# Kernel tuning notes

Hardware: AMD Instinct MI355X
Metric: run time of the kernel (lower is better)

The kernel has to match this reference:

```python
import jax, jax.numpy as jnp
import numpy as np

V, D, H, S = 100000, 300, 300, 4096   # vocab, embed dim, biLSTM hidden (2x150), seq len
HU = H // 2                            # per-direction LSTM units
NSYN = 4


def _lstm(x, W, U, b):
    """Keras-style LSTM scan. x: [S, D] -> hidden states [S, HU]. Gate order i,f,g,o."""
    def step(carry, xt):
        h, c = carry
        z = xt @ W + h @ U + b              # [4*HU]
        i, f, g, o = jnp.split(z, 4)
        i = jax.nn.sigmoid(i)
        f = jax.nn.sigmoid(f)
        g = jnp.tanh(g)
        o = jax.nn.sigmoid(o)
        c = f * c + i * g
        h = o * jnp.tanh(c)
        return (h, c), h
    init = (jnp.zeros((HU,), x.dtype), jnp.zeros((HU,), x.dtype))
    _, hs = jax.lax.scan(step, init, x)
    return hs


def setup_inputs() -> dict:
    key = jax.random.key(0)
    ks = jax.random.split(key, 20)
    s = 0.05  # small init scale keeps exp() attention scores well-conditioned
    return {
        "sentence": jax.random.randint(ks[0], (S,), 0, V),
        "synonym_indices": jax.random.randint(ks[1], (S, NSYN), 0, V),
        "embedding_matrix": jax.random.normal(ks[2], (V, D), jnp.float32) * s,
        # forward-direction LSTM
        "W_f": jax.random.normal(ks[3], (D, 4 * HU), jnp.float32) * s,
        "U_f": jax.random.normal(ks[4], (HU, 4 * HU), jnp.float32) * s,
        "b_f": jnp.zeros((4 * HU,), jnp.float32),
        # backward-direction LSTM
        "W_b": jax.random.normal(ks[5], (D, 4 * HU), jnp.float32) * s,
        "U_b": jax.random.normal(ks[6], (HU, 4 * HU), jnp.float32) * s,
        "b_b": jnp.zeros((4 * HU,), jnp.float32),
        # primary attention dense (h1 -> h1)
        "W_p": jax.random.normal(ks[7], (H, H), jnp.float32) * s,
        "b_p": jnp.zeros((H,), jnp.float32),
        # secondary attention dense (2*h1 -> 1, tanh)
        "W_s": jax.random.normal(ks[8], (2 * H, 1), jnp.float32) * s,
        "b_s": jnp.zeros((1,), jnp.float32),
        # output heads
        "W_emo": jax.random.normal(ks[9], (2 * H, 8), jnp.float32) * s,
        "b_emo": jnp.zeros((8,), jnp.float32),
        "W_sent": jax.random.normal(ks[10], (2 * H, 1), jnp.float32) * s,
        "b_sent": jnp.zeros((1,), jnp.float32),
    }


def reference(sentence, synonym_indices, embedding_matrix,
              W_f, U_f, b_f, W_b, U_b, b_b,
              W_p, b_p, W_s, b_s, W_emo, b_emo, W_sent, b_sent):
    emb = embedding_matrix[sentence]                       # [S, D] gather
    # bidirectional LSTM (concat fwd and reversed-bwd hidden states)
    h_fwd = _lstm(emb, W_f, U_f, b_f)                      # [S, HU]
    h_bwd = _lstm(emb[::-1], W_b, U_b, b_b)[::-1]          # [S, HU]
    hidden_states = jnp.concatenate([h_fwd, h_bwd], -1)    # [S, H]
    # primary attention: per-word synonym gather + exp-scored weighted sum (vectorized)
    out = hidden_states @ W_p + b_p                        # [S, H]
    syn = embedding_matrix[synonym_indices]                # [S, NSYN, D] irregular gather
    scores = jnp.exp(jnp.einsum('sd,skd->sk', out, syn))   # [S, NSYN]
    m = jnp.einsum('sk,skd->sd', scores, syn)              # [S, D]
    h_hats = jnp.concatenate([hidden_states, m], -1)       # [S, 2H]
    # secondary attention
    coeff = jnp.exp(jnp.tanh(h_hats @ W_s + b_s))          # [S, 1]
    H_HAT = jnp.sum(coeff * h_hats, axis=0)[None, :]       # [1, 2H]
    emotion_logits = H_HAT @ W_emo + b_emo                 # [1, 8]
    sentiment_logits = H_HAT @ W_sent + b_sent             # [1, 1]
    return (emotion_logits, sentiment_logits)
```

## Files before the change

### kernel.cpp

```cpp
#include <hip/hip_runtime.h>
#include <hip/hip_bf16.h>
#include <math.h>

#define S_LEN 4096
#define D_EMB 300
#define NG    600
#define HDIM  300
#define H2    600
#define VOCAB 100000

typedef float v4f __attribute__((ext_vector_type(4)));
typedef _Float16 f16x2 __attribute__((ext_vector_type(2)));
typedef _Float16 f16x8 __attribute__((ext_vector_type(8)));

__device__ __forceinline__ float bf2f(unsigned short u) {
  union { unsigned int i; float f; } v; v.i = ((unsigned int)u) << 16; return v.f;
}
__device__ __forceinline__ unsigned short f2bf(float f) {
  union { float f; unsigned int i; } v; v.f = f;
  return (unsigned short)((v.i + 0x7FFFu + ((v.i >> 16) & 1u)) >> 16);
}

__device__ __forceinline__ void bar_lds() {
  asm volatile("s_waitcnt lgkmcnt(0)\n\ts_barrier" ::: "memory");
}

__global__ void zero_hh(float* __restrict__ HH) {
  if (threadIdx.x < 640) HH[threadIdx.x] = 0.f;
}
__global__ void zero_out_f(float* __restrict__ o, int n) {
  if ((int)threadIdx.x < n) o[threadIdx.x] = 0.f;
}

#define BM 64
#define BN 64
#define BK 16
template<bool A_BF16>
__global__ __launch_bounds__(256) void gemm_bias(
    const void* __restrict__ Av,
    const int* __restrict__ idx, int lda, int nrowsA,
    const float* __restrict__ B,
    const float* __restrict__ bias,
    unsigned short* __restrict__ C,
    int N, int K)
{
  __shared__ __align__(16) float As[BK][BM + 4];
  __shared__ __align__(16) float Bs[BK][BN + 4];
  __shared__ int rowidx[BM];

  int tid = threadIdx.x;
  int bm0 = blockIdx.y * BM, bn0 = blockIdx.x * BN;
  if (tid < BM) {
    int r = idx ? idx[bm0 + tid] : (bm0 + tid);
    r = (r < 0) ? 0 : ((r >= nrowsA) ? (nrowsA - 1) : r);
    rowidx[tid] = r;
  }
  __syncthreads();

  int tx  = tid & 15, ty = tid >> 4;
  int ar  = tid >> 2, akv = (tid & 3) << 2;
  int bkr = tid >> 4, bnv = (tid & 15) << 2;

  float acc[4][4] = {};
  for (int kk = 0; kk < K; kk += BK) {
    float a0=0.f, a1=0.f, a2=0.f, a3=0.f;
    int ka = kk + akv;
    if (ka < K) {
      if (A_BF16) {
        const unsigned short* A = (const unsigned short*)Av;
        ushort4 qa = *(const ushort4*)(A + (size_t)rowidx[ar]*lda + ka);
        a0 = bf2f(qa.x); a1 = bf2f(qa.y); a2 = bf2f(qa.z); a3 = bf2f(qa.w);
      } else {
        const float* A = (const float*)Av;
        float4 qa = *(const float4*)(A + (size_t)rowidx[ar]*lda + ka);
        a0 = qa.x; a1 = qa.y; a2 = qa.z; a3 = qa.w;
      }
    }
    float b0=0.f, b1=0.f, b2=0.f, b3=0.f;
    int kb = kk + bkr, nb = bn0 + bnv;
    if (kb < K && nb < N) {
      float4 qb = *(const float4*)(B + (size_t)kb*N + nb);
      b0 = qb.x; b1 = qb.y; b2 = qb.z; b3 = qb.w;
    }
    As[akv+0][ar] = a0; As[akv+1][ar] = a1; As[akv+2][ar] = a2; As[akv+3][ar] = a3;
    Bs[bkr][bnv+0] = b0; Bs[bkr][bnv+1] = b1; Bs[bkr][bnv+2] = b2; Bs[bkr][bnv+3] = b3;
    __syncthreads();
    #pragma unroll
    for (int k = 0; k < BK; ++k) {
      v4f av = *(const v4f*)&As[k][ty << 2];
      v4f bv = *(const v4f*)&Bs[k][tx << 2];
      #pragma unroll
      for (int i = 0; i < 4; ++i)
        #pragma unroll
        for (int j = 0; j < 4; ++j)
          acc[i][j] += av[i] * bv[j];
    }
    __syncthreads();
  }
  #pragma unroll
  for (int i = 0; i < 4; ++i) {
    int m = bm0 + (ty << 2) + i;
    #pragma unroll
    for (int j = 0; j < 4; ++j) {
      int n = bn0 + (tx << 2) + j;
      if (n < N) C[(size_t)m*N + n] = f2bf(acc[i][j] + bias[n]);
    }
  }
}

__global__ __launch_bounds__(768) void lstm_kernel(
    const unsigned short* __restrict__ pre_f, const unsigned short* __restrict__ pre_b,
    const float* __restrict__ Uf, const float* __restrict__ Ub,
    unsigned short* __restrict__ hidden )
{
  const int dir = blockIdx.x;
  const unsigned short* pre = dir ? pre_b : pre_f;
  const float* U            = dir ? Ub : Uf;
  const int tid = threadIdx.x;

  __shared__ __align__(16) unsigned short h_u16[160];
  __shared__ __align__(16) float z2[3000];
  __shared__ __align__(16) float act[600];
  __shared__ __align__(16) float ring[3][600];
  __shared__ __align__(16) unsigned short h_hist[8][160];

  const bool faP = tid < 750;
  const int c4 = tid % 150, q = tid / 150;
  const int j0 = c4 << 2;
  const int k0 = q << 5;

  f16x2 u[4][16];
  if (faP) {
    #pragma unroll
    for (int cc = 0; cc < 4; ++cc)
      #pragma unroll
      for (int p = 0; p < 16; ++p) {
        int k = k0 + (p << 1);
        float a = (k     < 150) ? U[(size_t)k    *600 + j0 + cc] : 0.f;
        float b = (k + 1 < 150) ? U[(size_t)(k+1)*600 + j0 + cc] : 0.f;
        f16x2 v; v[0] = (_Float16)a; v[1] = (_Float16)b;
        u[cc][p] = v;
      }
  }

  int t  = dir ? (S_LEN - 1) : 0;
  const int dt = dir ? -1 : 1;

  if (tid < 160) h_u16[tid] = 0;
  unsigned short nxt1 = 0;
  if (tid < 600) {
    ring[0][tid] = bf2f(pre[(size_t)t*600 + tid]);
    nxt1 = pre[(size_t)(t + dt)*600 + tid];
  }
  float c = 0.f;
  __syncthreads();

  const _Float16* hf = (const _Float16*)h_u16;

  for (int s = 0; s < S_LEN; ++s) {
    if ((s & 7) == 0 && s) {
      if (tid < 600) {
        int sub = tid / 75, w = (tid % 75) << 1;
        int sp  = s - 8 + sub;
        int tp  = dir ? (S_LEN - 1 - sp) : sp;
        unsigned int v = *(const unsigned int*)&h_hist[sub][w];
        *(unsigned int*)(hidden + (size_t)tp*300 + dir*150 + w) = v;
      }
    }
    unsigned short nxt2 = 0;
    if (tid < 600 && s + 2 < S_LEN) nxt2 = pre[(size_t)(t + 2*dt)*600 + tid];

    if (faP) {
      f16x2 hp[16];
      *(f16x8*)&hp[0]  = *(const f16x8*)&hf[k0];
      *(f16x8*)&hp[4]  = *(const f16x8*)&hf[k0 + 8];
      *(f16x8*)&hp[8]  = *(const f16x8*)&hf[k0 + 16];
      *(f16x8*)&hp[12] = *(const f16x8*)&hf[k0 + 24];
      float a0 = 0.f, a1 = 0.f, a2 = 0.f, a3 = 0.f;
      #pragma unroll
      for (int p = 0; p < 16; ++p) {
        a0 = __builtin_amdgcn_fdot2(hp[p], u[0][p], a0, false);
        a1 = __builtin_amdgcn_fdot2(hp[p], u[1][p], a1, false);
        a2 = __builtin_amdgcn_fdot2(hp[p], u[2][p], a2, false);
        a3 = __builtin_amdgcn_fdot2(hp[p], u[3][p], a3, false);
      }
      v4f zp; zp[0] = a0; zp[1] = a1; zp[2] = a2; zp[3] = a3;
      *(v4f*)&z2[q*600 + j0] = zp;
    }
    if (tid < 600) ring[(s + 1) % 3][tid] = bf2f(nxt1);
    nxt1 = nxt2;
    bar_lds();

    if (tid < 600) {
      int j = tid;
      float z = ring[s % 3][j]
              + ((z2[j] + z2[600 + j]) + (z2[1200 + j] + z2[1800 + j]))
              + z2[2400 + j];
      bool is_g = (j >= 300) & (j < 450);
      float e = __expf(is_g ? (2.f * z) : (-z));
      float r = __builtin_amdgcn_rcpf(1.f + e);
      act[j] = is_g ? (1.f - 2.f * r) : r;
    }
    bar_lds();

    if (tid < 150) {
      float gi = act[tid], gf = act[150 + tid], gg = act[300 + tid], go = act[450 + tid];
      c = gf * c + gi * gg;
      float e = __expf(2.f * c);
      float th = 1.f - 2.f * __builtin_amdgcn_rcpf(e + 1.f);
      float hv = go * th;
      ((_Float16*)h_u16)[tid] = (_Float16)hv;
      h_hist[s & 7][tid] = f2bf(hv);
    }
    bar_lds();
    t += dt;
  }

  if (tid < 600) {
    int sub = tid / 75, w = (tid % 75) << 1;
    int sp  = S_LEN - 8 + sub;
    int tp  = dir ? (S_LEN - 1 - sp) : sp;
    unsigned int v = *(const unsigned int*)&h_hist[sub][w];
    *(unsigned int*)(hidden + (size_t)tp*300 + dir*150 + w) = v;
  }
}

__global__ __launch_bounds__(128) void attn_word(
    const unsigned short* __restrict__ outp,
    const unsigned short* __restrict__ hid,
    const float* __restrict__ E,
    const int* __restrict__ syn,
    const float* __restrict__ W_s,
    const float* __restrict__ b_s,
    float* __restrict__ HH)
{
  int t = blockIdx.x, tid = threadIdx.x;
  __shared__ float s_out[300], s_hid[300], s_syn[4][300], s_m[300];
  __shared__ float s_red[8], s_sc[4], s_cf;

  int r0 = syn[t*4+0], r1 = syn[t*4+1], r2 = syn[t*4+2], r3 = syn[t*4+3];
  r0 = (r0 < 0) ? 0 : ((r0 >= VOCAB) ? VOCAB-1 : r0);
  r1 = (r1 < 0) ? 0 : ((r1 >= VOCAB) ? VOCAB-1 : r1);
  r2 = (r2 < 0) ? 0 : ((r2 >= VOCAB) ? VOCAB-1 : r2);
  r3 = (r3 < 0) ? 0 : ((r3 >= VOCAB) ? VOCAB-1 : r3);
  for (int d = tid; d < 300; d += 128) {
    s_out[d] = bf2f(outp[(size_t)t*300 + d]);
    s_hid[d] = bf2f(hid[(size_t)t*300 + d]);
    s_syn[0][d] = E[(size_t)r0*300 + d];
    s_syn[1][d] = E[(size_t)r1*300 + d];
    s_syn[2][d] = E[(size_t)r2*300 + d];
    s_syn[3][d] = E[(size_t)r3*300 + d];
  }
  __syncthreads();

  float p0=0.f, p1=0.f, p2=0.f, p3=0.f;
  for (int d = tid; d < 300; d += 128) {
    float o = s_out[d];
    p0 += o*s_syn[0][d]; p1 += o*s_syn[1][d];
    p2 += o*s_syn[2][d]; p3 += o*s_syn[3][d];
  }
  #pragma unroll
  for (int off = 32; off; off >>= 1) {
    p0 += __shfl_down(p0, off); p1 += __shfl_down(p1, off);
    p2 += __shfl_down(p2, off); p3 += __shfl_down(p3, off);
  }
  int wave = tid >> 6, lane = tid & 63;
  if (lane == 0) {
    s_red[wave*4+0] = p0; s_red[wave*4+1] = p1;
    s_red[wave*4+2] = p2; s_red[wave*4+3] = p3;
  }
  __syncthreads();
  if (tid < 4) s_sc[tid] = __expf(fminf(s_red[tid] + s_red[4 + tid], 50.f));
  __syncthreads();

  float sc0 = s_sc[0], sc1 = s_sc[1], sc2 = s_sc[2], sc3 = s_sc[3];
  float cp = 0.f;
  for (int d = tid; d < 300; d += 128) {
    float m = sc0*s_syn[0][d] + sc1*s_syn[1][d] + sc2*s_syn[2][d] + sc3*s_syn[3][d];
    s_m[d] = m;
    cp += s_hid[d]*W_s[d] + m*W_s[300 + d];
  }
  #pragma unroll
  for (int off = 32; off; off >>= 1) cp += __shfl_down(cp, off);
  if (lane == 0) s_red[wave] = cp;
  __syncthreads();
  if (tid == 0) s_cf = __expf(tanhf(s_red[0] + s_red[1] + b_s[0]));
  __syncthreads();

  float cf = s_cf;
  for (int d = tid; d < 300; d += 128) {
    atomicAdd(&HH[d],       cf * s_hid[d]);
    atomicAdd(&HH[300 + d], cf * s_m[d]);
  }
}

__global__ void heads(const float* __restrict__ HH,
                      const float* __restrict__ W_emo, const float* __restrict__ b_emo,
                      const float* __restrict__ W_sent, const float* __restrict__ b_sent,
                      float* __restrict__ out) {
  int tid = threadIdx.x;
  if (tid < 8) {
    float a = 0.f;
    for (int d = 0; d < H2; ++d) a += HH[d] * W_emo[d*8 + tid];
    out[tid] = a + b_emo[tid];
  } else if (tid == 8) {
    float a = 0.f;
    for (int d = 0; d < H2; ++d) a += HH[d] * W_sent[d];
    out[8] = a + b_sent[0];
  }
}

extern "C" void kernel_launch(void* const* d_in, const int* in_sizes, int n_in,
                              void* d_out, int out_size, void* d_ws, size_t ws_size,
                              hipStream_t stream) {
  const int*   sentence = (const int*)d_in[0];
  const int*   syn_idx  = (const int*)d_in[1];
  const float* E        = (const float*)d_in[2];
  const float* W_f      = (const float*)d_in[3];
  const float* U_f      = (const float*)d_in[4];
  const float* b_f      = (const float*)d_in[5];
  const float* W_b      = (const float*)d_in[6];
  const float* U_b      = (const float*)d_in[7];
  const float* b_b      = (const float*)d_in[8];
  const float* W_p      = (const float*)d_in[9];
  const float* b_p      = (const float*)d_in[10];
  const float* W_s      = (const float*)d_in[11];
  const float* b_s      = (const float*)d_in[12];
  const float* W_emo    = (const float*)d_in[13];
  const float* b_emo    = (const float*)d_in[14];
  const float* W_sent   = (const float*)d_in[15];
  const float* b_sent   = (const float*)d_in[16];
  float*       outv     = (float*)d_out;

  unsigned char* ws = (unsigned char*)d_ws;
  float*          HH     = (float*)ws;
  unsigned short* hidden = (unsigned short*)(ws + 2560);
  unsigned short* out_p  = (unsigned short*)(ws + 2460160);
  unsigned short* pre_f  = (unsigned short*)(ws + 4917760);
  unsigned short* pre_b  = (unsigned short*)(ws + 9832960);

  if (ws_size < 14748160u) {
    zero_out_f<<<1, 64, 0, stream>>>(outv, out_size);
    return;
  }

  zero_hh<<<1, 640, 0, stream>>>(HH);
  gemm_bias<false><<<dim3(10, 64), 256, 0, stream>>>(
      (const void*)E, sentence, D_EMB, VOCAB, W_f, b_f, pre_f, NG, D_EMB);
  gemm_bias<false><<<dim3(10, 64), 256, 0, stream>>>(
      (const void*)E, sentence, D_EMB, VOCAB, W_b, b_b, pre_b, NG, D_EMB);
  lstm_kernel<<<2, 768, 0, stream>>>(pre_f, pre_b, U_f, U_b, hidden);
  gemm_bias<true><<<dim3(5, 64), 256, 0, stream>>>(
      (const void*)hidden, nullptr, HDIM, S_LEN, W_p, b_p, out_p, HDIM, HDIM);
  attn_word<<<S_LEN, 128, 0, stream>>>(out_p, hidden, E, syn_idx, W_s, b_s, HH);
  heads<<<1, 64, 0, stream>>>(HH, W_emo, b_emo, W_sent, b_sent, outv);
}
```

Measured before the change: 4.097 ms.

## Merge LSTM gate activation and cell update to drop a barrier per step

The gate-activation phase and the cell-update phase of the recurrent kernel are merged so that 150 threads each compute all four gate activations and the cell update for one unit. This removes one block-wide barrier per time step along with the act and ring LDS arrays. The precomputed input projections are now prefetched into registers two steps ahead, and the step loop is unrolled by 8 so the hidden-state flush sits outside the inner loop. The cost is more serial transcendental work per thread: each of the 150 active threads does five exp/rcp pairs where before 600 threads did one each. Only 150 of the 768 threads work in that phase.

```diff
diff --git a/kernel.cpp b/kernel.cpp
--- a/kernel.cpp
+++ b/kernel.cpp
@@ -120,11 +120,10 @@
 
   __shared__ __align__(16) unsigned short h_u16[160];
   __shared__ __align__(16) float z2[3000];
-  __shared__ __align__(16) float act[600];
-  __shared__ __align__(16) float ring[3][600];
   __shared__ __align__(16) unsigned short h_hist[8][160];
 
   const bool faP = tid < 750;
+  const bool bc  = tid < 150;
   const int c4 = tid % 150, q = tid / 150;
   const int j0 = c4 << 2;
   const int k0 = q << 5;
@@ -143,85 +142,90 @@
       }
   }
 
-  int t  = dir ? (S_LEN - 1) : 0;
+  const int t0 = dir ? (S_LEN - 1) : 0;
   const int dt = dir ? -1 : 1;
+  const ptrdiff_t pstep = (ptrdiff_t)dt * 600;
 
   if (tid < 160) h_u16[tid] = 0;
-  unsigned short nxt1 = 0;
-  if (tid < 600) {
-    ring[0][tid] = bf2f(pre[(size_t)t*600 + tid]);
-    nxt1 = pre[(size_t)(t + dt)*600 + tid];
+
+  float pA0=0,pA1=0,pA2=0,pA3=0, pB0=0,pB1=0,pB2=0,pB3=0;
+  const unsigned short* pre2 = pre + (ptrdiff_t)t0*600 + 2*pstep;
+  if (bc) {
+    const unsigned short* g0 = pre + (ptrdiff_t)t0*600;
+    pA0 = bf2f(g0[tid]); pA1 = bf2f(g0[tid+150]);
+    pA2 = bf2f(g0[tid+300]); pA3 = bf2f(g0[tid+450]);
+    const unsigned short* g1 = g0 + pstep;
+    pB0 = bf2f(g1[tid]); pB1 = bf2f(g1[tid+150]);
+    pB2 = bf2f(g1[tid+300]); pB3 = bf2f(g1[tid+450]);
   }
   float c = 0.f;
   __syncthreads();
 
   const _Float16* hf = (const _Float16*)h_u16;
 
-  for (int s = 0; s < S_LEN; ++s) {
-    if ((s & 7) == 0 && s) {
-      if (tid < 600) {
-        int sub = tid / 75, w = (tid % 75) << 1;
-        int sp  = s - 8 + sub;
-        int tp  = dir ? (S_LEN - 1 - sp) : sp;
-        unsigned int v = *(const unsigned int*)&h_hist[sub][w];
-        *(unsigned int*)(hidden + (size_t)tp*300 + dir*150 + w) = v;
-      }
-    }
-    unsigned short nxt2 = 0;
-    if (tid < 600 && s + 2 < S_LEN) nxt2 = pre[(size_t)(t + 2*dt)*600 + tid];
-
-    if (faP) {
-      f16x2 hp[16];
-      *(f16x8*)&hp[0]  = *(const f16x8*)&hf[k0];
-      *(f16x8*)&hp[4]  = *(const f16x8*)&hf[k0 + 8];
-      *(f16x8*)&hp[8]  = *(const f16x8*)&hf[k0 + 16];
-      *(f16x8*)&hp[12] = *(const f16x8*)&hf[k0 + 24];
-      float a0 = 0.f, a1 = 0.f, a2 = 0.f, a3 = 0.f;
-      #pragma unroll
-      for (int p = 0; p < 16; ++p) {
-        a0 = __builtin_amdgcn_fdot2(hp[p], u[0][p], a0, false);
-        a1 = __builtin_amdgcn_fdot2(hp[p], u[1][p], a1, false);
-        a2 = __builtin_amdgcn_fdot2(hp[p], u[2][p], a2, false);
-        a3 = __builtin_amdgcn_fdot2(hp[p], u[3][p], a3, false);
-      }
-      v4f zp; zp[0] = a0; zp[1] = a1; zp[2] = a2; zp[3] = a3;
-      *(v4f*)&z2[q*600 + j0] = zp;
-    }
-    if (tid < 600) ring[(s + 1) % 3][tid] = bf2f(nxt1);
-    nxt1 = nxt2;
-    bar_lds();
-
-    if (tid < 600) {
-      int j = tid;
-      float z = ring[s % 3][j]
-              + ((z2[j] + z2[600 + j]) + (z2[1200 + j] + z2[1800 + j]))
-              + z2[2400 + j];
-      bool is_g = (j >= 300) & (j < 450);
-      float e = __expf(is_g ? (2.f * z) : (-z));
-      float r = __builtin_amdgcn_rcpf(1.f + e);
-      act[j] = is_g ? (1.f - 2.f * r) : r;
-    }
-    bar_lds();
-
-    if (tid < 150) {
-      float gi = act[tid], gf = act[150 + tid], gg = act[300 + tid], go = act[450 + tid];
-      c = gf * c + gi * gg;
-      float e = __expf(2.f * c);
-      float th = 1.f - 2.f * __builtin_amdgcn_rcpf(e + 1.f);
-      float hv = go * th;
-      ((_Float16*)h_u16)[tid] = (_Float16)hv;
-      h_hist[s & 7][tid] = f2bf(hv);
-    }
-    bar_lds();
-    t += dt;
+  for (int s8 = 0; s8 < S_LEN/8; ++s8) {
+    if (s8 && tid < 600) {
+      int sub = tid / 75, w = (tid % 75) << 1;
+      int sp  = (s8 << 3) - 8 + sub;
+      int tp  = dir ? (S_LEN - 1 - sp) : sp;
+      *(unsigned int*)(hidden + (size_t)tp*300 + dir*150 + w) =
+          *(const unsigned int*)&h_hist[sub][w];
+    }
+    #pragma unroll
+    for (int ss = 0; ss < 8; ++ss) {
+      const int s = (s8 << 3) + ss;
+      if (faP) {
+        f16x2 hp[16];
+        *(f16x8*)&hp[0]  = *(const f16x8*)&hf[k0];
+        *(f16x8*)&hp[4]  = *(const f16x8*)&hf[k0 + 8];
+        *(f16x8*)&hp[8]  = *(const f16x8*)&hf[k0 + 16];
+        *(f16x8*)&hp[12] = *(const f16x8*)&hf[k0 + 24];
+        float a0 = 0.f, a1 = 0.f, a2 = 0.f, a3 = 0.f;
+        #pragma unroll
+        for (int p = 0; p < 16; ++p) {
+          a0 = __builtin_amdgcn_fdot2(hp[p], u[0][p], a0, false);
+          a1 = __builtin_amdgcn_fdot2(hp[p], u[1][p], a1, false);
+          a2 = __builtin_amdgcn_fdot2(hp[p], u[2][p], a2, false);
+          a3 = __builtin_amdgcn_fdot2(hp[p], u[3][p], a3, false);
+        }
+        v4f zp; zp[0] = a0; zp[1] = a1; zp[2] = a2; zp[3] = a3;
+        *(v4f*)&z2[q*600 + j0] = zp;
+      }
+      float pC0=0,pC1=0,pC2=0,pC3=0;
+      if (bc && s + 2 < S_LEN) {
+        pC0 = bf2f(pre2[tid]);       pC1 = bf2f(pre2[tid+150]);
+        pC2 = bf2f(pre2[tid+300]);   pC3 = bf2f(pre2[tid+450]);
+      }
+      bar_lds();
+
+      if (bc) {
+        float zi = pA0 + ((z2[tid      ] + z2[600+tid      ]) + (z2[1200+tid      ] + z2[1800+tid      ])) + z2[2400+tid      ];
+        float zf = pA1 + ((z2[tid + 150] + z2[600+tid + 150]) + (z2[1200+tid + 150] + z2[1800+tid + 150])) + z2[2400+tid + 150];
+        float zg = pA2 + ((z2[tid + 300] + z2[600+tid + 300]) + (z2[1200+tid + 300] + z2[1800+tid + 300])) + z2[2400+tid + 300];
+        float zo = pA3 + ((z2[tid + 450] + z2[600+tid + 450]) + (z2[1200+tid + 450] + z2[1800+tid + 450])) + z2[2400+tid + 450];
+        float gi = __builtin_amdgcn_rcpf(1.f + __expf(-zi));
+        float gf = __builtin_amdgcn_rcpf(1.f + __expf(-zf));
+        float gg = 1.f - 2.f * __builtin_amdgcn_rcpf(__expf(2.f * zg) + 1.f);
+        float go = __builtin_amdgcn_rcpf(1.f + __expf(-zo));
+        c = gf * c + gi * gg;
+        float th = 1.f - 2.f * __builtin_amdgcn_rcpf(__expf(2.f * c) + 1.f);
+        float hv = go * th;
+        ((_Float16*)h_u16)[tid] = (_Float16)hv;
+        h_hist[ss][tid] = f2bf(hv);
+        pA0 = pB0; pA1 = pB1; pA2 = pB2; pA3 = pB3;
+        pB0 = pC0; pB1 = pC1; pB2 = pC2; pB3 = pC3;
+      }
+      bar_lds();
+      pre2 += pstep;
+    }
   }
 
   if (tid < 600) {
     int sub = tid / 75, w = (tid % 75) << 1;
     int sp  = S_LEN - 8 + sub;
     int tp  = dir ? (S_LEN - 1 - sp) : sp;
-    unsigned int v = *(const unsigned int*)&h_hist[sub][w];
-    *(unsigned int*)(hidden + (size_t)tp*300 + dir*150 + w) = v;
+    *(unsigned int*)(hidden + (size_t)tp*300 + dir*150 + w) =
+        *(const unsigned int*)&h_hist[sub][w];
   }
 }
 
```

Result: faster. 3.621 ms (-11.6%).
